# Optimization experiments

Measured on AMD Instinct MI355X. Metric: run time of the kernel, lower is better.

The kernel has to match this reference:

```python
import jax, jax.numpy as jnp
import numpy as np
import math

GROUPS = 32
HEADS = 8
EPS = 1e-5


def group_norm(x, w, b):
    B, C, H, W = x.shape
    xg = x.reshape(B, GROUPS, C // GROUPS, H, W)
    mu = xg.mean(axis=(2, 3, 4), keepdims=True)
    var = xg.var(axis=(2, 3, 4), keepdims=True)
    xg = (xg - mu) * jax.lax.rsqrt(var + EPS)
    return xg.reshape(B, C, H, W) * w[None, :, None, None] + b[None, :, None, None]


def setup_inputs() -> dict:
    key = jax.random.key(0)
    ks = jax.random.split(key, 3)
    C = 512
    x = jax.random.normal(ks[0], (4, C, 64, 64), dtype=jnp.float32)
    norm_w = jnp.ones((C,), dtype=jnp.float32)
    norm_b = jnp.zeros((C,), dtype=jnp.float32)
    qkv_w = jax.random.normal(ks[1], (3 * C, C), dtype=jnp.float32) * 0.02
    qkv_b = jnp.zeros((3 * C,), dtype=jnp.float32)
    proj_w = jax.random.normal(ks[2], (C, C), dtype=jnp.float32) * 0.02
    proj_b = jnp.zeros((C,), dtype=jnp.float32)
    return {"x": x, "norm_w": norm_w, "norm_b": norm_b, "qkv_w": qkv_w,
            "qkv_b": qkv_b, "proj_w": proj_w, "proj_b": proj_b}


def reference(x, norm_w, norm_b, qkv_w, qkv_b, proj_w, proj_b):
    B, C, H, W = x.shape
    S = H * W
    head_dim = C // HEADS
    scale = 1.0 / math.sqrt(head_dim)

    h = group_norm(x, norm_w, norm_b)
    # 1x1 conv == pointwise linear over channels
    qkv = jnp.einsum('oc,bchw->bohw', qkv_w, h) + qkv_b[None, :, None, None]
    q, k, v = jnp.split(qkv, 3, axis=1)
    q = q.reshape(B, HEADS, head_dim, S)
    k = k.reshape(B, HEADS, head_dim, S)
    v = v.reshape(B, HEADS, head_dim, S)

    # chunked softmax attention in the original is row-wise softmax, i.e.
    # mathematically identical to full attention over all queries
    attn = jnp.einsum('bhdi,bhdj->bhij', q, k) * scale  # [B,H,S,S]
    attn = jax.nn.softmax(attn, axis=-1)
    out = jnp.einsum('bhij,bhdj->bhdi', attn, v)  # [B,H,d,S]

    out = out.reshape(B, C, H, W)
    out = jnp.einsum('oc,bchw->bohw', proj_w, out) + proj_b[None, :, None, None]
    return out + x
```

## Files before the change

kernel.cpp:

```cpp
#include <hip/hip_runtime.h>
#include <hip/hip_bf16.h>

#define NB 4
#define NC 512
#define NS 4096
#define NH 8
#define HD 64
#define NG 32
#define CPG 16
#define QKC 1024
#define CQF 0.18033688f

typedef __attribute__((ext_vector_type(8))) short bf16x8;
typedef __attribute__((ext_vector_type(4))) float f32x4;
typedef __attribute__((ext_vector_type(16))) float f32x16;

__device__ __forceinline__ unsigned short f2bf(float f) {
  union { float f; unsigned int u; } v; v.f = f;
  unsigned int r = v.u + 0x7FFFu + ((v.u >> 16) & 1u);
  return (unsigned short)(r >> 16);
}

__device__ __forceinline__ unsigned short f2bf_rn(float f) {
  union { __hip_bfloat16 h; unsigned short u; } cv;
  cv.h = __float2bfloat16(f);
  return cv.u;
}

__device__ __forceinline__ void gload16(const unsigned short* g, unsigned short* s) {
  __builtin_amdgcn_global_load_lds(
      (const __attribute__((address_space(1))) unsigned int*)g,
      (__attribute__((address_space(3))) unsigned int*)s, 16, 0, 0);
}

__global__ __launch_bounds__(256) void prep_k(const float* __restrict__ x,
                                              float* __restrict__ pstats,
                                              const float* __restrict__ wq,
                                              const float* __restrict__ wp,
                                              unsigned short* __restrict__ wqb,
                                              unsigned short* __restrict__ wpb) {
  int bid = blockIdx.x;
  if (bid < NB * NG * 4) {
    int bgq = bid;
    const float4* xp = (const float4*)(x + (size_t)bgq * (CPG * NS / 4));
    float s = 0.f, s2 = 0.f;
    #pragma unroll 4
    for (int i = threadIdx.x; i < CPG * NS / 16; i += 256) {
      float4 v = xp[i];
      s  += v.x + v.y + v.z + v.w;
      s2 += v.x * v.x + v.y * v.y + v.z * v.z + v.w * v.w;
    }
    #pragma unroll
    for (int off = 32; off > 0; off >>= 1) {
      s  += __shfl_down(s, off);
      s2 += __shfl_down(s2, off);
    }
    __shared__ float rs[4], rs2[4];
    int wid = threadIdx.x >> 6;
    if ((threadIdx.x & 63) == 0) { rs[wid] = s; rs2[wid] = s2; }
    __syncthreads();
    if (threadIdx.x == 0) {
      pstats[bgq * 2]     = rs[0] + rs[1] + rs[2] + rs[3];
      pstats[bgq * 2 + 1] = rs2[0] + rs2[1] + rs2[2] + rs2[3];
    }
  } else {
    const int nq8 = 3 * NC * NC / 8, np8 = NC * NC / 8, se8 = NC * NC / 8;
    int i = (bid - NB * NG * 4) * 256 + threadIdx.x;
    if (i >= nq8 + np8) return;
    const float* src;
    unsigned short* dst;
    float sc;
    int j;
    if (i < nq8) { src = wq; dst = wqb; j = i; sc = (i < se8) ? CQF : 1.0f; }
    else         { src = wp; dst = wpb; j = i - nq8; sc = 1.0f; }
    const float4* s = (const float4*)src + (size_t)j * 2;
    float4 a = s[0], b = s[1];
    ushort4 u0 = make_ushort4(f2bf_rn(a.x * sc), f2bf_rn(a.y * sc),
                              f2bf_rn(a.z * sc), f2bf_rn(a.w * sc));
    ushort4 u1 = make_ushort4(f2bf_rn(b.x * sc), f2bf_rn(b.y * sc),
                              f2bf_rn(b.z * sc), f2bf_rn(b.w * sc));
    uint4 o;
    o.x = (unsigned)u0.x | ((unsigned)u0.y << 16);
    o.y = (unsigned)u0.z | ((unsigned)u0.w << 16);
    o.z = (unsigned)u1.x | ((unsigned)u1.y << 16);
    o.w = (unsigned)u1.z | ((unsigned)u1.w << 16);
    *((uint4*)dst + j) = o;
  }
}

__global__ __launch_bounds__(256) void gn_apply_k(const float* __restrict__ x,
                                                  const float* __restrict__ pstats,
                                                  const float* __restrict__ nw,
                                                  const float* __restrict__ nb,
                                                  unsigned short* __restrict__ ht) {
  int st = blockIdx.x, ct = blockIdx.y, b = blockIdx.z;
  int c0 = ct * 64, s0 = st * 64;
  __shared__ unsigned short lds[64][72];
  for (int idx = threadIdx.x; idx < 1024; idx += 256) {
    int row = idx >> 4, c4 = idx & 15;
    int c = c0 + row;
    int gi = (b * NG + (c >> 4)) * 4;
    const float4* pq = (const float4*)(pstats + gi * 2);
    float4 p01 = pq[0], p23 = pq[1];
    float sum = p01.x + p01.z + p23.x + p23.z;
    float ssq = p01.y + p01.w + p23.y + p23.w;
    float inv_n = 1.0f / (CPG * NS);
    float mu = sum * inv_n;
    float var = ssq * inv_n - mu * mu;
    float rstd = rsqrtf(var + 1e-5f);
    float sw = nw[c] * rstd;
    float sb = nb[c] - mu * sw;
    float4 v = *(const float4*)(x + ((size_t)b * NC + c) * NS + s0 + c4 * 4);
    ushort4 u = make_ushort4(f2bf(v.x * sw + sb), f2bf(v.y * sw + sb),
                             f2bf(v.z * sw + sb), f2bf(v.w * sw + sb));
    *(ushort4*)&lds[row][c4 * 4] = u;
  }
  __syncthreads();
  for (int idx = threadIdx.x; idx < 1024; idx += 256) {
    int i = idx >> 4, ch = idx & 15;
    ushort4 u = make_ushort4(lds[ch * 4 + 0][i], lds[ch * 4 + 1][i],
                             lds[ch * 4 + 2][i], lds[ch * 4 + 3][i]);
    *(ushort4*)(ht + ((size_t)b * NS + s0 + i) * NC + c0 + ch * 4) = u;
  }
}

__global__ __launch_bounds__(256) void qkv_gemm_k(const unsigned short* __restrict__ ht,
                                                  const unsigned short* __restrict__ wqb,
                                                  const float* __restrict__ bq,
                                                  unsigned short* __restrict__ qk,
                                                  unsigned short* __restrict__ vt) {
  int b = blockIdx.z;
  int m0 = blockIdx.x * 128, n0 = blockIdx.y * 128;
  __shared__ unsigned short alds[128 * 64];
  __shared__ unsigned short blds[128 * 64];
  const unsigned short* A = ht + (size_t)b * NS * NC;
  int tid = threadIdx.x;
  int l = tid & 63, w = tid >> 6;
  int wr = w >> 1, wc = w & 1;
  int lm = l & 15, lg = l >> 4;
  int lrow = l >> 3, lcb = l & 7;
  f32x4 acc[4][4];
  #pragma unroll
  for (int mi = 0; mi < 4; mi++)
    #pragma unroll
    for (int ni = 0; ni < 4; ni++) acc[mi][ni] = (f32x4){0.f, 0.f, 0.f, 0.f};

  for (int k0 = 0; k0 < NC; k0 += 64) {
    #pragma unroll
    for (int j = 0; j < 4; j++) {
      int row = w * 32 + j * 8 + lrow;
      int scb = lcb ^ (row & 7);
      gload16(A   + (size_t)(m0 + row) * NC + k0 + scb * 8, &alds[(w * 4 + j) * 512]);
      gload16(wqb + (size_t)(n0 + row) * NC + k0 + scb * 8, &blds[(w * 4 + j) * 512]);
    }
    __syncthreads();
    #pragma unroll
    for (int ks = 0; ks < 2; ks++) {
      bf16x8 af[4], bfr[4];
      #pragma unroll
      for (int mi = 0; mi < 4; mi++) {
        int row = wr * 64 + mi * 16 + lm;
        af[mi] = *(const bf16x8*)&alds[((row << 6) + (ks << 5) + (lg << 3)) ^ ((row & 7) << 3)];
      }
      #pragma unroll
      for (int ni = 0; ni < 4; ni++) {
        int row = wc * 64 + ni * 16 + lm;
        bfr[ni] = *(const bf16x8*)&blds[((row << 6) + (ks << 5) + (lg << 3)) ^ ((row & 7) << 3)];
      }
      #pragma unroll
      for (int mi = 0; mi < 4; mi++)
        #pragma unroll
        for (int ni = 0; ni < 4; ni++)
          acc[mi][ni] = __builtin_amdgcn_mfma_f32_16x16x32_bf16(af[mi], bfr[ni], acc[mi][ni], 0, 0, 0);
    }
    __syncthreads();
  }
  if (n0 < QKC) {
    #pragma unroll
    for (int mi = 0; mi < 4; mi++) {
      #pragma unroll
      for (int ni = 0; ni < 4; ni++) {
        int o = n0 + wc * 64 + ni * 16 + lm;
        float bias = bq[o];
        if (o < NC) bias *= CQF;
        #pragma unroll
        for (int q = 0; q < 4; q++) {
          int s = m0 + wr * 64 + mi * 16 + lg * 4 + q;
          qk[((size_t)b * NS + s) * QKC + o] = f2bf(acc[mi][ni][q] + bias);
        }
      }
    }
  } else {
    #pragma unroll
    for (int mi = 0; mi < 4; mi++) {
      int s0 = m0 + wr * 64 + mi * 16 + lg * 4;
      #pragma unroll
      for (int ni = 0; ni < 4; ni++) {
        int o = n0 + wc * 64 + ni * 16 + lm;
        float bias = bq[o];
        int dg = o - QKC;
        ushort4 u = make_ushort4(f2bf(acc[mi][ni][0] + bias), f2bf(acc[mi][ni][1] + bias),
                                 f2bf(acc[mi][ni][2] + bias), f2bf(acc[mi][ni][3] + bias));
        *(ushort4*)(vt + ((size_t)b * NC + dg) * NS + s0) = u;
      }
    }
  }
}

__global__ __launch_bounds__(512) void attn_k(const unsigned short* __restrict__ qk,
                                              const unsigned short* __restrict__ vt,
                                              unsigned short* __restrict__ ob) {
  int bid = blockIdx.x;
  int xcd = bid & 7, g = bid >> 3;
  int pair = xcd * 4 + (g >> 4);
  int qt = g & 15;
  int h = pair & 7, b = pair >> 3;
  int tid = threadIdx.x;
  int l = tid & 63, w = tid >> 6;
  int l31 = l & 31, hi = l >> 5;
  __shared__ unsigned short slds[24576];
  const unsigned short* qkb = qk + (size_t)b * NS * QKC;
  const unsigned short* vtb = vt + ((size_t)b * NC + h * HD) * NS;
  int iw = qt * 256 + w * 32;

  bf16x8 fq[4];
  #pragma unroll
  for (int kk = 0; kk < 4; kk++)
    fq[kk] = *(const bf16x8*)(qkb + (size_t)(iw + l31) * QKC + h * HD + kk * 16 + hi * 8);

  bf16x8 ones;
  #pragma unroll
  for (int e = 0; e < 8; e++) ones[e] = (short)0x3F80;

  int rb = (((l31 << 6) + (hi << 3)) ^ ((l31 & 7) << 3));
  int rbk[4] = { rb, rb ^ 16, rb ^ 32, rb ^ 48 };

  int kr = w * 8 + (l >> 3);
  int scb = (l & 7) ^ (l >> 3);
  const unsigned short* kgp = qkb + NC + h * HD + (size_t)kr * QKC + scb * 8;
  const unsigned short* vgp = vtb + (size_t)kr * NS + scb * 8;
  unsigned short* kd0 = &slds[w * 512];
  unsigned short* kd1 = kd0 + 8192;
  unsigned short* kd2 = kd0 + 16384;
  unsigned short* vd0 = &slds[4096 + w * 512];
  unsigned short* vd1 = vd0 + 8192;
  unsigned short* vd2 = vd0 + 16384;

  f32x16 acc_o0 = {}, acc_o1 = {}, acc_l = {};

  bf16x8 vA[8], vB[8], pA[4], pB[4];
  #pragma unroll
  for (int e = 0; e < 8; e++) vB[e] = (bf16x8){0, 0, 0, 0, 0, 0, 0, 0};
  #pragma unroll
  for (int e = 0; e < 4; e++) pB[e] = (bf16x8){0, 0, 0, 0, 0, 0, 0, 0};

  gload16(kgp, kd0); gload16(vgp, vd0);
  kgp += (size_t)64 * QKC; vgp += 64;
  gload16(kgp, kd1); gload16(vgp, vd1);
  kgp += (size_t)64 * QKC; vgp += 64;
  asm volatile("s_waitcnt vmcnt(2)" ::: "memory");
  __builtin_amdgcn_s_barrier();

  #define CVTSW(SA, q, DST) {                                                       \
    unsigned X0, X1, Y0, Y1;                                                        \
    asm("v_cvt_pk_bf16_f32 %0, %1, %2" : "=v"(X0) : "v"(SA[q*8+0]), "v"(SA[q*8+1]));\
    asm("v_cvt_pk_bf16_f32 %0, %1, %2" : "=v"(X1) : "v"(SA[q*8+2]), "v"(SA[q*8+3]));\
    asm("v_cvt_pk_bf16_f32 %0, %1, %2" : "=v"(Y0) : "v"(SA[q*8+4]), "v"(SA[q*8+5]));\
    asm("v_cvt_pk_bf16_f32 %0, %1, %2" : "=v"(Y1) : "v"(SA[q*8+6]), "v"(SA[q*8+7]));\
    asm("v_permlane32_swap_b32 %0, %1" : "+v"(X0), "+v"(Y0));                       \
    asm("v_permlane32_swap_b32 %0, %1" : "+v"(X1), "+v"(Y1));                       \
    union { unsigned u[4]; bf16x8 v; } pu = {{X0, X1, Y0, Y1}};                     \
    DST = pu.v; }

  #define TILE(RB, IB, WC, VN, VP, PN, PP) {                                        \
    if (WC) {                                                                       \
      gload16(kgp, kd##IB); gload16(vgp, vd##IB);                                   \
      kgp += (size_t)64 * QKC; vgp += 64;                                           \
    }                                                                               \
    const unsigned short* Kr = &slds[(RB)*8192];                                    \
    const unsigned short* Vr = &slds[(RB)*8192 + 4096];                             \
    f32x16 sa0 = {}, sa1 = {};                                                      \
    __builtin_amdgcn_s_setprio(1);                                                  \
    _Pragma("unroll")                                                               \
    for (int kk = 0; kk < 4; kk++) {                                                \
      bf16x8 ak = *(const bf16x8*)&Kr[rbk[kk]];                                     \
      sa0 = __builtin_amdgcn_mfma_f32_32x32x16_bf16(ak, fq[kk], sa0, 0, 0, 0);      \
    }                                                                               \
    _Pragma("unroll")                                                               \
    for (int kk = 0; kk < 4; kk++) {                                                \
      bf16x8 ak = *(const bf16x8*)&Kr[rbk[kk] + 2048];                              \
      sa1 = __builtin_amdgcn_mfma_f32_32x32x16_bf16(ak, fq[kk], sa1, 0, 0, 0);      \
    }                                                                               \
    _Pragma("unroll")                                                               \
    for (int kk = 0; kk < 4; kk++) {                                                \
      VN[kk]     = *(const bf16x8*)&Vr[rbk[kk]];                                    \
      VN[kk + 4] = *(const bf16x8*)&Vr[rbk[kk] + 2048];                             \
    }                                                                               \
    _Pragma("unroll")                                                               \
    for (int bq_ = 0; bq_ < 4; bq_++) {                                             \
      acc_l  = __builtin_amdgcn_mfma_f32_32x32x16_bf16(PP[bq_], ones, acc_l, 0, 0, 0);        \
      acc_o0 = __builtin_amdgcn_mfma_f32_32x32x16_bf16(PP[bq_], VP[bq_], acc_o0, 0, 0, 0);    \
      acc_o1 = __builtin_amdgcn_mfma_f32_32x32x16_bf16(PP[bq_], VP[bq_ + 4], acc_o1, 0, 0, 0);\
    }                                                                               \
    __builtin_amdgcn_s_setprio(0);                                                  \
    _Pragma("unroll")                                                               \
    for (int r = 0; r < 16; r++) {                                                  \
      sa0[r] = __builtin_amdgcn_exp2f(sa0[r]);                                      \
      sa1[r] = __builtin_amdgcn_exp2f(sa1[r]);                                      \
    }                                                                               \
    CVTSW(sa0, 0, PN[0]);                                                           \
    CVTSW(sa0, 1, PN[1]);                                                           \
    CVTSW(sa1, 0, PN[2]);                                                           \
    CVTSW(sa1, 1, PN[3]);                                                           \
    if (WC) asm volatile("s_waitcnt vmcnt(2) lgkmcnt(0)" ::: "memory");             \
    else    asm volatile("s_waitcnt vmcnt(0) lgkmcnt(0)" ::: "memory");             \
    __builtin_amdgcn_s_barrier(); }

  for (int it = 0; it < 10; ++it) {
    TILE(0, 2, 2, vA, vB, pA, pB)
    TILE(1, 0, 2, vB, vA, pB, pA)
    TILE(2, 1, 2, vA, vB, pA, pB)
    TILE(0, 2, 2, vB, vA, pB, pA)
    TILE(1, 0, 2, vA, vB, pA, pB)
    TILE(2, 1, 2, vB, vA, pB, pA)
  }
  TILE(0, 2, 2, vA, vB, pA, pB)
  TILE(1, 0, 2, vB, vA, pB, pA)
  TILE(2, 0, 0, vA, vB, pA, pB)
  TILE(0, 0, 0, vB, vA, pB, pA)
  #undef TILE
  #undef CVTSW

  #pragma unroll
  for (int bq_ = 0; bq_ < 4; bq_++) {
    acc_l  = __builtin_amdgcn_mfma_f32_32x32x16_bf16(pB[bq_], ones, acc_l, 0, 0, 0);
    acc_o0 = __builtin_amdgcn_mfma_f32_32x32x16_bf16(pB[bq_], vB[bq_], acc_o0, 0, 0, 0);
    acc_o1 = __builtin_amdgcn_mfma_f32_32x32x16_bf16(pB[bq_], vB[bq_ + 4], acc_o1, 0, 0, 0);
  }

  #pragma unroll
  for (int r = 0; r < 16; r++) {
    float inv = __builtin_amdgcn_rcpf(acc_l[r]);
    int i = (r & 3) + 8 * (r >> 2) + 4 * hi;
    size_t rowo = ((size_t)b * NS + (iw + i)) * NC + h * HD;
    ob[rowo + l31]      = f2bf_rn(acc_o0[r] * inv);
    ob[rowo + 32 + l31] = f2bf_rn(acc_o1[r] * inv);
  }
}

__global__ __launch_bounds__(256) void proj_gemm_k(const unsigned short* __restrict__ wpb,
                                                   const float* __restrict__ bp,
                                                   const unsigned short* __restrict__ obuf,
                                                   const float* __restrict__ x,
                                                   float* __restrict__ out) {
  int b = blockIdx.z;
  int m0 = blockIdx.x * 128, n0 = blockIdx.y * 128;
  __shared__ unsigned short alds[128 * 64];
  __shared__ unsigned short blds[128 * 64];
  const unsigned short* Bt = obuf + (size_t)b * NS * NC;
  int tid = threadIdx.x;
  int l = tid & 63, w = tid >> 6;
  int wr = w >> 1, wc = w & 1;
  int lm = l & 15, lg = l >> 4;
  int lrow = l >> 3, lcb = l & 7;
  f32x4 acc[4][4];
  #pragma unroll
  for (int mi = 0; mi < 4; mi++)
    #pragma unroll
    for (int ni = 0; ni < 4; ni++) acc[mi][ni] = (f32x4){0.f, 0.f, 0.f, 0.f};

  for (int k0 = 0; k0 < NC; k0 += 64) {
    #pragma unroll
    for (int j = 0; j < 4; j++) {
      int row = w * 32 + j * 8 + lrow;
      int scb = lcb ^ (row & 7);
      gload16(wpb + (size_t)(m0 + row) * NC + k0 + scb * 8, &alds[(w * 4 + j) * 512]);
      gload16(Bt  + (size_t)(n0 + row) * NC + k0 + scb * 8, &blds[(w * 4 + j) * 512]);
    }
    __syncthreads();
    #pragma unroll
    for (int ks = 0; ks < 2; ks++) {
      bf16x8 af[4], bfr[4];
      #pragma unroll
      for (int mi = 0; mi < 4; mi++) {
        int row = wr * 64 + mi * 16 + lm;
        af[mi] = *(const bf16x8*)&alds[((row << 6) + (ks << 5) + (lg << 3)) ^ ((row & 7) << 3)];
      }
      #pragma unroll
      for (int ni = 0; ni < 4; ni++) {
        int row = wc * 64 + ni * 16 + lm;
        bfr[ni] = *(const bf16x8*)&blds[((row << 6) + (ks << 5) + (lg << 3)) ^ ((row & 7) << 3)];
      }
      #pragma unroll
      for (int mi = 0; mi < 4; mi++)
        #pragma unroll
        for (int ni = 0; ni < 4; ni++)
          acc[mi][ni] = __builtin_amdgcn_mfma_f32_16x16x32_bf16(af[mi], bfr[ni], acc[mi][ni], 0, 0, 0);
    }
    __syncthreads();
  }
  #pragma unroll
  for (int mi = 0; mi < 4; mi++) {
    #pragma unroll
    for (int q = 0; q < 4; q++) {
      int o = m0 + wr * 64 + mi * 16 + lg * 4 + q;
      float bias = bp[o];
      #pragma unroll
      for (int ni = 0; ni < 4; ni++) {
        int s = n0 + wc * 64 + ni * 16 + lm;
        size_t idx = ((size_t)b * NC + o) * NS + s;
        out[idx] = acc[mi][ni][q] + bias + x[idx];
      }
    }
  }
}

extern "C" void kernel_launch(void* const* d_in, const int* in_sizes, int n_in,
                              void* d_out, int out_size, void* d_ws, size_t ws_size,
                              hipStream_t stream) {
  const float* x  = (const float*)d_in[0];
  const float* nw = (const float*)d_in[1];
  const float* nb = (const float*)d_in[2];
  const float* wq = (const float*)d_in[3];
  const float* bq = (const float*)d_in[4];
  const float* wp = (const float*)d_in[5];
  const float* bp = (const float*)d_in[6];
  float* out = (float*)d_out;

  char* ws = (char*)d_ws;
  size_t off = 0;
  off += 1024;
  unsigned short* ht  = (unsigned short*)(ws + off); off += (size_t)NB * NS * NC * 2;
  unsigned short* qk  = (unsigned short*)(ws + off); off += (size_t)NB * NS * QKC * 2;
  unsigned short* vt  = (unsigned short*)(ws + off); off += (size_t)NB * NS * NC * 2;
  unsigned short* wqb = (unsigned short*)(ws + off); off += (size_t)3 * NC * NC * 2;
  unsigned short* wpb = (unsigned short*)(ws + off); off += (size_t)NC * NC * 2;
  unsigned short* ob  = ht;
  float* pstats = (float*)qk;

  prep_k<<<dim3(1024), 256, 0, stream>>>(x, pstats, wq, wp, wqb, wpb);
  gn_apply_k<<<dim3(NS / 64, NC / 64, NB), 256, 0, stream>>>(x, pstats, nw, nb, ht);
  qkv_gemm_k<<<dim3(NS / 128, 1536 / 128, NB), 256, 0, stream>>>(ht, wqb, bq, qk, vt);
  attn_k<<<dim3(512), 512, 0, stream>>>(qk, vt, ob);
  proj_gemm_k<<<dim3(NC / 128, NS / 128, NB), 256, 0, stream>>>(wpb, bp, ob, x, out);
}
```

Measured before the change: 220.5 us.

## Read V from LDS at PV time via 4-stage buffer, drop V register prefetch

The attention kernel no longer stages the next V tile into registers (vA/vB, 16 bf16x8 vectors). Instead, LDS grows from three to four K/V buffers, so the previous tile's V stays resident and is read straight from shared memory inside the PV MFMA loop. The unused fourth V buffer is zeroed so the first PV step is correct. Launch bounds now request 4 waves per SIMD, aiming to cut VGPR pressure and raise occupancy. The cost is more LDS per block and LDS reads on the PV critical path, which may stall the MFMAs.

```diff
diff --git a/kernel.cpp b/kernel.cpp
--- a/kernel.cpp
+++ b/kernel.cpp
@@ -207,9 +207,9 @@
   }
 }
 
-__global__ __launch_bounds__(512) void attn_k(const unsigned short* __restrict__ qk,
-                                              const unsigned short* __restrict__ vt,
-                                              unsigned short* __restrict__ ob) {
+__global__ __launch_bounds__(512, 4) void attn_k(const unsigned short* __restrict__ qk,
+                                                 const unsigned short* __restrict__ vt,
+                                                 unsigned short* __restrict__ ob) {
   int bid = blockIdx.x;
   int xcd = bid & 7, g = bid >> 3;
   int pair = xcd * 4 + (g >> 4);
@@ -218,7 +218,7 @@
   int tid = threadIdx.x;
   int l = tid & 63, w = tid >> 6;
   int l31 = l & 31, hi = l >> 5;
-  __shared__ unsigned short slds[24576];
+  __shared__ unsigned short slds[32768];
   const unsigned short* qkb = qk + (size_t)b * NS * QKC;
   const unsigned short* vtb = vt + ((size_t)b * NC + h * HD) * NS;
   int iw = qt * 256 + w * 32;
@@ -239,26 +239,22 @@
   int scb = (l & 7) ^ (l >> 3);
   const unsigned short* kgp = qkb + NC + h * HD + (size_t)kr * QKC + scb * 8;
   const unsigned short* vgp = vtb + (size_t)kr * NS + scb * 8;
-  unsigned short* kd0 = &slds[w * 512];
-  unsigned short* kd1 = kd0 + 8192;
-  unsigned short* kd2 = kd0 + 16384;
-  unsigned short* vd0 = &slds[4096 + w * 512];
-  unsigned short* vd1 = vd0 + 8192;
-  unsigned short* vd2 = vd0 + 16384;
+  unsigned short* kdls = &slds[w * 512];
+  unsigned short* vdls = &slds[4096 + w * 512];
 
   f32x16 acc_o0 = {}, acc_o1 = {}, acc_l = {};
 
-  bf16x8 vA[8], vB[8], pA[4], pB[4];
-  #pragma unroll
-  for (int e = 0; e < 8; e++) vB[e] = (bf16x8){0, 0, 0, 0, 0, 0, 0, 0};
+  bf16x8 pA[4], pB[4];
   #pragma unroll
   for (int e = 0; e < 4; e++) pB[e] = (bf16x8){0, 0, 0, 0, 0, 0, 0, 0};
 
-  gload16(kgp, kd0); gload16(vgp, vd0);
+  *(uint4*)&slds[3 * 8192 + 4096 + tid * 8] = (uint4){0, 0, 0, 0};
+
+  gload16(kgp, kdls); gload16(vgp, vdls);
   kgp += (size_t)64 * QKC; vgp += 64;
-  gload16(kgp, kd1); gload16(vgp, vd1);
+  gload16(kgp, kdls + 8192); gload16(vgp, vdls + 8192);
   kgp += (size_t)64 * QKC; vgp += 64;
-  asm volatile("s_waitcnt vmcnt(2)" ::: "memory");
+  asm volatile("s_waitcnt vmcnt(2) lgkmcnt(0)" ::: "memory");
   __builtin_amdgcn_s_barrier();
 
   #define CVTSW(SA, q, DST) {                                                       \
@@ -272,13 +268,13 @@
     union { unsigned u[4]; bf16x8 v; } pu = {{X0, X1, Y0, Y1}};                     \
     DST = pu.v; }
 
-  #define TILE(RB, IB, WC, VN, VP, PN, PP) {                                        \
+  #define TILE(RB, IB, PVB, WC, PN, PP) {                                           \
     if (WC) {                                                                       \
-      gload16(kgp, kd##IB); gload16(vgp, vd##IB);                                   \
+      gload16(kgp, kdls + (IB) * 8192); gload16(vgp, vdls + (IB) * 8192);           \
       kgp += (size_t)64 * QKC; vgp += 64;                                           \
     }                                                                               \
-    const unsigned short* Kr = &slds[(RB)*8192];                                    \
-    const unsigned short* Vr = &slds[(RB)*8192 + 4096];                             \
+    const unsigned short* Kr = &slds[(RB) * 8192];                                  \
+    const unsigned short* Vp = &slds[(PVB) * 8192 + 4096];                          \
     f32x16 sa0 = {}, sa1 = {};                                                      \
     __builtin_amdgcn_s_setprio(1);                                                  \
     _Pragma("unroll")                                                               \
@@ -292,15 +288,12 @@
       sa1 = __builtin_amdgcn_mfma_f32_32x32x16_bf16(ak, fq[kk], sa1, 0, 0, 0);      \
     }                                                                               \
     _Pragma("unroll")                                                               \
-    for (int kk = 0; kk < 4; kk++) {                                                \
-      VN[kk]     = *(const bf16x8*)&Vr[rbk[kk]];                                    \
-      VN[kk + 4] = *(const bf16x8*)&Vr[rbk[kk] + 2048];                             \
-    }                                                                               \
-    _Pragma("unroll")                                                               \
     for (int bq_ = 0; bq_ < 4; bq_++) {                                             \
-      acc_l  = __builtin_amdgcn_mfma_f32_32x32x16_bf16(PP[bq_], ones, acc_l, 0, 0, 0);        \
-      acc_o0 = __builtin_amdgcn_mfma_f32_32x32x16_bf16(PP[bq_], VP[bq_], acc_o0, 0, 0, 0);    \
-      acc_o1 = __builtin_amdgcn_mfma_f32_32x32x16_bf16(PP[bq_], VP[bq_ + 4], acc_o1, 0, 0, 0);\
+      bf16x8 bv0 = *(const bf16x8*)&Vp[rbk[bq_]];                                   \
+      bf16x8 bv1 = *(const bf16x8*)&Vp[rbk[bq_] + 2048];                            \
+      acc_l  = __builtin_amdgcn_mfma_f32_32x32x16_bf16(PP[bq_], ones, acc_l, 0, 0, 0);    \
+      acc_o0 = __builtin_amdgcn_mfma_f32_32x32x16_bf16(PP[bq_], bv0, acc_o0, 0, 0, 0);    \
+      acc_o1 = __builtin_amdgcn_mfma_f32_32x32x16_bf16(PP[bq_], bv1, acc_o1, 0, 0, 0);    \
     }                                                                               \
     __builtin_amdgcn_s_setprio(0);                                                  \
     _Pragma("unroll")                                                               \
@@ -316,26 +309,29 @@
     else    asm volatile("s_waitcnt vmcnt(0) lgkmcnt(0)" ::: "memory");             \
     __builtin_amdgcn_s_barrier(); }
 
-  for (int it = 0; it < 10; ++it) {
-    TILE(0, 2, 2, vA, vB, pA, pB)
-    TILE(1, 0, 2, vB, vA, pB, pA)
-    TILE(2, 1, 2, vA, vB, pA, pB)
-    TILE(0, 2, 2, vB, vA, pB, pA)
-    TILE(1, 0, 2, vA, vB, pA, pB)
-    TILE(2, 1, 2, vB, vA, pB, pA)
-  }
-  TILE(0, 2, 2, vA, vB, pA, pB)
-  TILE(1, 0, 2, vB, vA, pB, pA)
-  TILE(2, 0, 0, vA, vB, pA, pB)
-  TILE(0, 0, 0, vB, vA, pB, pA)
+  for (int it = 0; it < 15; ++it) {
+    TILE(0, 2, 3, 1, pA, pB)
+    TILE(1, 3, 0, 1, pB, pA)
+    TILE(2, 0, 1, 1, pA, pB)
+    TILE(3, 1, 2, 1, pB, pA)
+  }
+  TILE(0, 2, 3, 1, pA, pB)
+  TILE(1, 3, 0, 1, pB, pA)
+  TILE(2, 0, 1, 0, pA, pB)
+  TILE(3, 0, 2, 0, pB, pA)
   #undef TILE
   #undef CVTSW
 
-  #pragma unroll
-  for (int bq_ = 0; bq_ < 4; bq_++) {
-    acc_l  = __builtin_amdgcn_mfma_f32_32x32x16_bf16(pB[bq_], ones, acc_l, 0, 0, 0);
-    acc_o0 = __builtin_amdgcn_mfma_f32_32x32x16_bf16(pB[bq_], vB[bq_], acc_o0, 0, 0, 0);
-    acc_o1 = __builtin_amdgcn_mfma_f32_32x32x16_bf16(pB[bq_], vB[bq_ + 4], acc_o1, 0, 0, 0);
+  {
+    const unsigned short* Vp = &slds[3 * 8192 + 4096];
+    #pragma unroll
+    for (int bq_ = 0; bq_ < 4; bq_++) {
+      bf16x8 bv0 = *(const bf16x8*)&Vp[rbk[bq_]];
+      bf16x8 bv1 = *(const bf16x8*)&Vp[rbk[bq_] + 2048];
+      acc_l  = __builtin_amdgcn_mfma_f32_32x32x16_bf16(pB[bq_], ones, acc_l, 0, 0, 0);
+      acc_o0 = __builtin_amdgcn_mfma_f32_32x32x16_bf16(pB[bq_], bv0, acc_o0, 0, 0, 0);
+      acc_o1 = __builtin_amdgcn_mfma_f32_32x32x16_bf16(pB[bq_], bv1, acc_o1, 0, 0, 0);
+    }
   }
 
   #pragma unroll
```

After: 406.1 us. 1.84x slower.
